# Performance work log

Hardware: AMD Instinct MI355X
Metric: run time of the kernel (lower is better)

## Reference

```python
import jax, jax.numpy as jnp
import numpy as np

EMBED_DIM = 768
NUM_HEADS = 12
HEAD_DIM = EMBED_DIM // NUM_HEADS
SCALE = HEAD_DIM ** -0.5
EPS = 1e-5


def _layernorm(x, g, b):
    m = jnp.mean(x, axis=-1, keepdims=True)
    v = jnp.mean(jnp.square(x - m), axis=-1, keepdims=True)
    return (x - m) * jax.lax.rsqrt(v + EPS) * g + b


def setup_inputs() -> dict:
    key = jax.random.key(0)
    ks = jax.random.split(key, 8)
    B, N, D, Hd = 16, 1024, EMBED_DIM, HEAD_DIM
    x = jax.random.normal(ks[0], (B, N, D), dtype=jnp.float32)
    W_qkv = jax.random.normal(ks[1], (D, 3 * D), dtype=jnp.float32) * (D ** -0.5)
    b_qkv = jnp.zeros((3 * D,), dtype=jnp.float32)
    W_proj = jax.random.normal(ks[2], (D, D), dtype=jnp.float32) * (D ** -0.5)
    b_proj = jnp.zeros((D,), dtype=jnp.float32)
    return {
        "x": x,
        "ln_g": jnp.ones((D,), jnp.float32), "ln_b": jnp.zeros((D,), jnp.float32),
        "W_qkv": W_qkv, "b_qkv": b_qkv,
        "qn_g": jnp.ones((Hd,), jnp.float32), "qn_b": jnp.zeros((Hd,), jnp.float32),
        "kn_g": jnp.ones((Hd,), jnp.float32), "kn_b": jnp.zeros((Hd,), jnp.float32),
        "W_proj": W_proj, "b_proj": b_proj,
    }


def reference(x, ln_g, ln_b, W_qkv, b_qkv, qn_g, qn_b, kn_g, kn_b, W_proj, b_proj):
    B, N, D = x.shape
    H, Hd = NUM_HEADS, HEAD_DIM
    xn = _layernorm(x, ln_g, ln_b)                      # qkv_norm (pre-LN of embed_dim)
    qkv = xn @ W_qkv + b_qkv                            # [B,N,3D]
    qkv = qkv.reshape(B, N, 3, H, Hd)
    q = jnp.transpose(qkv[:, :, 0], (0, 2, 1, 3))       # [B,H,N,Hd]
    k = jnp.transpose(qkv[:, :, 1], (0, 2, 1, 3))
    v = jnp.transpose(qkv[:, :, 2], (0, 2, 1, 3))
    q = _layernorm(q, qn_g, qn_b)                       # per-head QK LayerNorm
    k = _layernorm(k, kn_g, kn_b)
    attn = jnp.einsum("bhnd,bhmd->bhnm", q, k) * SCALE
    attn = jax.nn.softmax(attn, axis=-1)
    out = jnp.einsum("bhnm,bhmd->bhnd", attn, v)        # [B,H,N,Hd]
    out = jnp.transpose(out, (0, 2, 1, 3)).reshape(B, N, D)
    return out @ W_proj + b_proj
```

## Files before the change

kernel.cpp:

```cpp
#include <hip/hip_runtime.h>

typedef _Float16 half8 __attribute__((ext_vector_type(8)));
typedef _Float16 half4 __attribute__((ext_vector_type(4)));
typedef _Float16 half2v __attribute__((ext_vector_type(2)));
typedef float f32x4 __attribute__((ext_vector_type(4)));

#define B_    16
#define N_    1024
#define D_    768
#define H_    12
#define M_    (B_ * N_)
#define QKVN_ 2304
#define EPS_  1e-5f
#define QS_   0.18033688011112042f

__device__ __forceinline__ float exp2_fast(float x) {
#if __has_builtin(__builtin_amdgcn_exp2f)
    return __builtin_amdgcn_exp2f(x);
#else
    return __builtin_exp2f(x);
#endif
}

__device__ __forceinline__ size_t pk(int t16, int kc, int lg, int p, int e) {
    return ((size_t)(t16 * 24 + kc) * 4 + lg) * 128 + p * 8 + e;
}

__global__ __launch_bounds__(256) void convert_w(const float* __restrict__ Wqkv,
                                                 const float* __restrict__ Wproj,
                                                 _Float16* __restrict__ wqkv_p,
                                                 _Float16* __restrict__ wproj_p) {
    __shared__ float T[64][65];
    int t = blockIdx.x;
    const float* W; _Float16* O; int NW, k0, n0;
    if (t < 432) { W = Wqkv;  O = wqkv_p;  NW = QKVN_; k0 = (t % 12) * 64; n0 = (t / 12) * 64; }
    else { t -= 432; W = Wproj; O = wproj_p; NW = D_;  k0 = (t % 12) * 64; n0 = (t / 12) * 64; }
    int c = threadIdx.x & 63, r4 = threadIdx.x >> 6;
#pragma unroll
    for (int i = 0; i < 16; ++i) {
        int k = i * 4 + r4;
        T[c][k] = W[(size_t)(k0 + k) * NW + n0 + c];
    }
    __syncthreads();
    int g = threadIdx.x >> 5, s2 = threadIdx.x & 31;
    int ntl = g & 3, kcl = g >> 2;
    int nt = (n0 >> 4) + ntl, kc = (k0 >> 5) + kcl;
#pragma unroll
    for (int hh = 0; hh < 2; ++hh) {
        int s = s2 + hh * 32;
        int lg = s >> 4, p = s & 15;
        half8 v;
#pragma unroll
        for (int e = 0; e < 8; ++e)
            v[e] = (_Float16)T[ntl * 16 + p][kcl * 32 + lg * 8 + e];
        *(half8*)&O[((size_t)(nt * 24 + kc) * 4 + lg) * 128 + p * 8] = v;
    }
}

__global__ __launch_bounds__(256) void ln_embed(const float* __restrict__ x,
                                                const float* __restrict__ g,
                                                const float* __restrict__ bb,
                                                _Float16* __restrict__ xp) {
    int row = blockIdx.x;
    int tid = threadIdx.x;
    const float2* xr = (const float2*)(x + (size_t)row * D_);
    float2 v0 = xr[tid];
    float2 v1 = make_float2(0.f, 0.f);
    if (tid < 128) v1 = xr[256 + tid];
    float s = v0.x + v0.y + v1.x + v1.y;
    float q = v0.x * v0.x + v0.y * v0.y + v1.x * v1.x + v1.y * v1.y;
#pragma unroll
    for (int m = 32; m >= 1; m >>= 1) {
        s += __shfl_xor(s, m);
        q += __shfl_xor(q, m);
    }
    __shared__ float ss[4], qq[4];
    int wave = tid >> 6;
    if ((tid & 63) == 0) { ss[wave] = s; qq[wave] = q; }
    __syncthreads();
    float S = ss[0] + ss[1] + ss[2] + ss[3];
    float Q = qq[0] + qq[1] + qq[2] + qq[3];
    float mean = S * (1.f / 768.f);
    float var  = Q * (1.f / 768.f) - mean * mean;
    float rstd = rsqrtf(var + EPS_);
    const float2* g2 = (const float2*)g;
    const float2* b2 = (const float2*)bb;
    int mt = row >> 4, p = row & 15;
    {
        int d0 = 2 * tid;
        float2 ga = g2[tid], ba = b2[tid];
        half2v w;
        w[0] = (_Float16)((v0.x - mean) * rstd * ga.x + ba.x);
        w[1] = (_Float16)((v0.y - mean) * rstd * ga.y + ba.y);
        *(half2v*)&xp[pk(mt, d0 >> 5, (d0 >> 3) & 3, p, d0 & 7)] = w;
    }
    if (tid < 128) {
        int d0 = 512 + 2 * tid;
        float2 ga = g2[256 + tid], ba = b2[256 + tid];
        half2v w;
        w[0] = (_Float16)((v1.x - mean) * rstd * ga.x + ba.x);
        w[1] = (_Float16)((v1.y - mean) * rstd * ga.y + ba.y);
        *(half2v*)&xp[pk(mt, d0 >> 5, (d0 >> 3) & 3, p, d0 & 7)] = w;
    }
}

__global__ __launch_bounds__(256, 3) void gemm_qkv(const _Float16* __restrict__ Ap,
                                                   const _Float16* __restrict__ Bp,
                                                   const float* __restrict__ bias,
                                                   const float* __restrict__ qn_g,
                                                   const float* __restrict__ qn_b,
                                                   const float* __restrict__ kn_g,
                                                   const float* __restrict__ kn_b,
                                                   _Float16* __restrict__ qo,
                                                   _Float16* __restrict__ ko,
                                                   _Float16* __restrict__ vt) {
    int xcd = blockIdx.x & 7, loc = blockIdx.x >> 3;
    int mt0 = (xcd * 16 + (loc & 15)) * 8;
    int nt0 = (loc >> 4) * 8;
    int tid = threadIdx.x;
    int wave = tid >> 6, lane = tid & 63;
    int wm = wave >> 1, wn = wave & 1;
    int lg = lane >> 4, l15 = lane & 15;

    const _Float16* pa[4];
    const _Float16* pb[4];
#pragma unroll
    for (int i = 0; i < 4; ++i) {
        pa[i] = Ap + (size_t)(mt0 + wm * 4 + i) * 12288 + lane * 8;
        pb[i] = Bp + (size_t)(nt0 + wn * 4 + i) * 12288 + lane * 8;
    }
    f32x4 acc[4][4] = {};
    half8 a0[4], b0[4], a1[4], b1[4], a2[4], b2[4];
    auto ld = [&](half8 (&a)[4], half8 (&b)[4], int t) {
        int off = t * 512;
#pragma unroll
        for (int i = 0; i < 4; ++i) {
            a[i] = *(const half8*)(pa[i] + off);
            b[i] = *(const half8*)(pb[i] + off);
        }
    };
    auto mm = [&](half8 (&a)[4], half8 (&b)[4]) {
#pragma unroll
        for (int mi = 0; mi < 4; ++mi)
#pragma unroll
            for (int ni = 0; ni < 4; ++ni)
                acc[mi][ni] = __builtin_amdgcn_mfma_f32_16x16x32_f16(a[mi], b[ni], acc[mi][ni], 0, 0, 0);
    };
    ld(a0, b0, 0); ld(a1, b1, 1);
    for (int tt = 0; tt < 8; ++tt) {
        ld(a2, b2, 3 * tt + 2);
        mm(a0, b0);
        if (tt < 7) ld(a0, b0, 3 * tt + 3);
        mm(a1, b1);
        if (tt < 7) ld(a1, b1, 3 * tt + 4);
        mm(a2, b2);
    }

    int m0 = mt0 * 16, n0 = nt0 * 16;
    int col0 = n0 + wn * 64;
    int s = col0 / 768;
    int hcol = (col0 % 768) >> 6;
    float qkvb[4];
#pragma unroll
    for (int ni = 0; ni < 4; ++ni) qkvb[ni] = bias[col0 + ni * 16 + l15];

    if (s == 2) {
#pragma unroll
        for (int mi = 0; mi < 4; ++mi) {
            int r0 = m0 + wm * 64 + mi * 16 + lg * 4;
            int bidx = r0 >> 10, pos = r0 & 1023;
            int kvblk = pos >> 5, h = (pos >> 4) & 1, lgR = (pos >> 2) & 3;
            size_t vbase = ((size_t)(bidx * H_ + hcol) * 32 + kvblk) * 4;
#pragma unroll
            for (int ni = 0; ni < 4; ++ni) {
                half4 h4;
#pragma unroll
                for (int j = 0; j < 4; ++j) h4[j] = (_Float16)(acc[mi][ni][j] + qkvb[ni]);
                *(half4*)&vt[(vbase + ni) * 512 + lgR * 128 + l15 * 8 + h * 4] = h4;
            }
        }
    } else {
        const float* gg = (s == 0) ? qn_g : kn_g;
        const float* bb = (s == 0) ? qn_b : kn_b;
        float gv[4], bv[4];
#pragma unroll
        for (int ni = 0; ni < 4; ++ni) { gv[ni] = gg[ni * 16 + l15]; bv[ni] = bb[ni * 16 + l15]; }
#pragma unroll
        for (int mi = 0; mi < 4; ++mi) {
#pragma unroll
            for (int j = 0; j < 4; ++j) {
                float v[4];
                float sm = 0.f, sq = 0.f;
#pragma unroll
                for (int ni = 0; ni < 4; ++ni) {
                    v[ni] = acc[mi][ni][j] + qkvb[ni];
                    sm += v[ni];
                    sq += v[ni] * v[ni];
                }
#pragma unroll
                for (int msk = 1; msk < 16; msk <<= 1) {
                    sm += __shfl_xor(sm, msk);
                    sq += __shfl_xor(sq, msk);
                }
                float mean = sm * (1.f / 64.f);
                float var  = sq * (1.f / 64.f) - mean * mean;
                float rstd = rsqrtf(var + EPS_);
                int row = m0 + wm * 64 + mi * 16 + lg * 4 + j;
                int bidx = row >> 10, pos = row & 1023;
                if (s == 0) {
                    size_t rbase = ((size_t)(bidx * H_ + hcol) * 1024 + pos) * 64;
#pragma unroll
                    for (int ni = 0; ni < 4; ++ni) {
                        float o = (v[ni] - mean) * rstd * gv[ni] + bv[ni];
                        qo[rbase + ni * 16 + l15] = (_Float16)(o * QS_);
                    }
                } else {
                    int kvblk = pos >> 5, nh = (pos >> 4) & 1, l15R = pos & 15;
                    size_t base2 = ((size_t)(bidx * H_ + hcol) * 32 + kvblk) * 4 + nh * 2;
#pragma unroll
                    for (int ni = 0; ni < 4; ++ni) {
                        float o = (v[ni] - mean) * rstd * gv[ni] + bv[ni];
                        int ks = ni >> 1, lgR = ((ni & 1) << 1) | (l15 >> 3), elem = l15 & 7;
                        ko[(base2 + ks) * 512 + lgR * 128 + l15R * 8 + elem] = (_Float16)o;
                    }
                }
            }
        }
    }
}

struct KV {
    half8 kf[2][2];
    half8 vf[4];
};

__device__ __forceinline__ void ldKV(KV& s, const _Float16* kp, const _Float16* vp, int kvblk) {
    const _Float16* kb = kp + (size_t)kvblk * 2048;
#pragma unroll
    for (int nh = 0; nh < 2; ++nh)
#pragma unroll
        for (int ks = 0; ks < 2; ++ks)
            s.kf[nh][ks] = *(const half8*)(kb + (nh * 2 + ks) * 512);
    const _Float16* vb = vp + (size_t)kvblk * 2048;
#pragma unroll
    for (int di = 0; di < 4; ++di)
        s.vf[di] = *(const half8*)(vb + di * 512);
}

__device__ __forceinline__ void blockKV(const KV& s, const half8 (&qf)[4][2],
                                        f32x4 (&oacc)[4][4], f32x4 (&lacc)[4],
                                        half8 ones) {
#pragma unroll
    for (int mi = 0; mi < 4; ++mi) {
        f32x4 a0 = {}, a1 = {};
#pragma unroll
        for (int ks = 0; ks < 2; ++ks) {
            a0 = __builtin_amdgcn_mfma_f32_16x16x32_f16(s.kf[0][ks], qf[mi][ks], a0, 0, 0, 0);
            a1 = __builtin_amdgcn_mfma_f32_16x16x32_f16(s.kf[1][ks], qf[mi][ks], a1, 0, 0, 0);
        }
        half8 pf;
#pragma unroll
        for (int j = 0; j < 4; ++j) {
            pf[j]     = (_Float16)exp2_fast(a0[j]);
            pf[j + 4] = (_Float16)exp2_fast(a1[j]);
        }
        lacc[mi] = __builtin_amdgcn_mfma_f32_16x16x32_f16(ones, pf, lacc[mi], 0, 0, 0);
#pragma unroll
        for (int di = 0; di < 4; ++di)
            oacc[mi][di] = __builtin_amdgcn_mfma_f32_16x16x32_f16(s.vf[di], pf, oacc[mi][di], 0, 0, 0);
    }
}

__global__ __launch_bounds__(128, 2) void attn(const _Float16* __restrict__ qg,
                                               const _Float16* __restrict__ kg,
                                               const _Float16* __restrict__ vtg,
                                               _Float16* __restrict__ op) {
    int bphys = blockIdx.x;
    int jj = (bphys & 7) * 192 + (bphys >> 3);
    int bh = jj >> 3, qt = jj & 7;
    int b = bh / H_, h = bh % H_;
    int tid = threadIdx.x;
    int wid = tid >> 6, lane = tid & 63;
    int lg = lane >> 4, l15 = lane & 15;
    size_t base = (size_t)bh << 10;
    int qw0 = qt * 128 + wid * 64;

    const _Float16* qrow = qg + (base + qw0 + l15) * 64 + lg * 8;
    half8 qf[4][2];
#pragma unroll
    for (int mi = 0; mi < 4; ++mi)
#pragma unroll
        for (int ks = 0; ks < 2; ++ks)
            qf[mi][ks] = *(const half8*)(qrow + mi * 1024 + ks * 32);

    const _Float16* kp = kg + (size_t)bh * 65536 + lane * 8;
    const _Float16* vp = vtg + (size_t)bh * 65536 + lane * 8;

    half8 ones;
#pragma unroll
    for (int i = 0; i < 8; ++i) ones[i] = (_Float16)1.0f;

    f32x4 oacc[4][4] = {};
    f32x4 lacc[4] = {};

    KV s0, s1;
    ldKV(s0, kp, vp, 0);
    for (int t = 0; t < 16; ++t) {
        ldKV(s1, kp, vp, (2 * t + 1) & 31);
        blockKV(s0, qf, oacc, lacc, ones);
        ldKV(s0, kp, vp, (2 * t + 2) & 31);
        blockKV(s1, qf, oacc, lacc, ones);
    }

#pragma unroll
    for (int mi = 0; mi < 4; ++mi) {
        float inv = 1.f / lacc[mi][0];
        int mt = b * 64 + (qw0 >> 4) + mi;
#pragma unroll
        for (int di = 0; di < 4; ++di) {
            half4 h4;
#pragma unroll
            for (int j = 0; j < 4; ++j) h4[j] = (_Float16)(oacc[mi][di][j] * inv);
            *(half4*)&op[pk(mt, 2 * h + (di >> 1), (di & 1) * 2 + (lg >> 1), l15, (lg & 1) * 4)] = h4;
        }
    }
}

__global__ __launch_bounds__(256, 3) void gemm_proj(const _Float16* __restrict__ Ap,
                                                    const _Float16* __restrict__ Bp,
                                                    const float* __restrict__ bias,
                                                    float* __restrict__ out) {
    int xcd = blockIdx.x & 7, loc = blockIdx.x >> 3;
    int mt0 = (xcd * 16 + (loc & 15)) * 8;
    int nt0 = (loc >> 4) * 8;
    int tid = threadIdx.x;
    int wave = tid >> 6, lane = tid & 63;
    int wm = wave >> 1, wn = wave & 1;
    int lg = lane >> 4, l15 = lane & 15;

    const _Float16* pa[4];
    const _Float16* pb[4];
#pragma unroll
    for (int i = 0; i < 4; ++i) {
        pa[i] = Ap + (size_t)(mt0 + wm * 4 + i) * 12288 + lane * 8;
        pb[i] = Bp + (size_t)(nt0 + wn * 4 + i) * 12288 + lane * 8;
    }
    f32x4 acc[4][4] = {};
    half8 a0[4], b0[4], a1[4], b1[4], a2[4], b2[4];
    auto ld = [&](half8 (&a)[4], half8 (&b)[4], int t) {
        int off = t * 512;
#pragma unroll
        for (int i = 0; i < 4; ++i) {
            a[i] = *(const half8*)(pa[i] + off);
            b[i] = *(const half8*)(pb[i] + off);
        }
    };
    auto mm = [&](half8 (&a)[4], half8 (&b)[4]) {
#pragma unroll
        for (int mi = 0; mi < 4; ++mi)
#pragma unroll
            for (int ni = 0; ni < 4; ++ni)
                acc[mi][ni] = __builtin_amdgcn_mfma_f32_16x16x32_f16(a[mi], b[ni], acc[mi][ni], 0, 0, 0);
    };
    ld(a0, b0, 0); ld(a1, b1, 1);
    for (int tt = 0; tt < 8; ++tt) {
        ld(a2, b2, 3 * tt + 2);
        mm(a0, b0);
        if (tt < 7) ld(a0, b0, 3 * tt + 3);
        mm(a1, b1);
        if (tt < 7) ld(a1, b1, 3 * tt + 4);
        mm(a2, b2);
    }

    int m0 = mt0 * 16, n0 = nt0 * 16;
#pragma unroll
    for (int mi = 0; mi < 4; ++mi)
#pragma unroll
        for (int ni = 0; ni < 4; ++ni) {
            int col = n0 + wn * 64 + ni * 16 + l15;
            float bv = bias[col];
#pragma unroll
            for (int j = 0; j < 4; ++j) {
                int row = m0 + wm * 64 + mi * 16 + lg * 4 + j;
                out[(size_t)row * D_ + col] = acc[mi][ni][j] + bv;
            }
        }
}

extern "C" void kernel_launch(void* const* d_in, const int* in_sizes, int n_in,
                              void* d_out, int out_size, void* d_ws, size_t ws_size,
                              hipStream_t stream) {
    const float* x      = (const float*)d_in[0];
    const float* ln_g   = (const float*)d_in[1];
    const float* ln_b   = (const float*)d_in[2];
    const float* W_qkv  = (const float*)d_in[3];
    const float* b_qkv  = (const float*)d_in[4];
    const float* qn_g   = (const float*)d_in[5];
    const float* qn_b   = (const float*)d_in[6];
    const float* kn_g   = (const float*)d_in[7];
    const float* kn_b   = (const float*)d_in[8];
    const float* W_proj = (const float*)d_in[9];
    const float* b_proj = (const float*)d_in[10];
    float* out = (float*)d_out;
    char* ws = (char*)d_ws;

    constexpr size_t XN_SZ    = (size_t)M_ * D_ * 2;
    constexpr size_t WQKVT_SZ = (size_t)QKVN_ * D_ * 2;
    constexpr size_t WPROJT_SZ= (size_t)D_ * D_ * 2;
    constexpr size_t HEAD_SZ  = (size_t)B_ * H_ * N_ * 64 * 2;

    _Float16* xn_p   = (_Float16*)(ws);
    _Float16* wqkv_p = (_Float16*)(ws + XN_SZ);
    _Float16* wproj_p= (_Float16*)(ws + XN_SZ + WQKVT_SZ);
    _Float16* qb     = (_Float16*)(ws + XN_SZ + WQKVT_SZ + WPROJT_SZ);
    _Float16* kb     = (_Float16*)((char*)qb + HEAD_SZ);
    _Float16* vtb    = (_Float16*)((char*)kb + HEAD_SZ);
    _Float16* ao_p   = xn_p;

    convert_w<<<576, 256, 0, stream>>>(W_qkv, W_proj, wqkv_p, wproj_p);
    ln_embed<<<M_, 256, 0, stream>>>(x, ln_g, ln_b, xn_p);
    gemm_qkv<<<M_ / 128 * (QKVN_ / 128), 256, 0, stream>>>(xn_p, wqkv_p, b_qkv,
                                                           qn_g, qn_b, kn_g, kn_b,
                                                           qb, kb, vtb);
    attn<<<B_ * H_ * (N_ / 128), 128, 0, stream>>>(qb, kb, vtb, ao_p);
    gemm_proj<<<M_ / 128 * (D_ / 128), 256, 0, stream>>>(ao_p, wproj_p, b_proj, out);
}
```

Baseline: 201.6 us.

## Stage GEMM tiles through LDS with async global-to-LDS loads and triple buffering

Both GEMMs move from per-wave direct global loads to 256x128 block tiles staged in shared memory through global_load_lds, with a three-buffer pipeline, explicit barriers and vmcnt waits. Each block now has 8 waves, so A and B fragments are loaded once and shared across waves rather than fetched by every wave from global memory. The activation and weight packed layouts are reorganised into 64-wide K tiles so each staging copy is contiguous, and the writers (LN, attention output, weight conversion) are changed to match. The hand-scheduled waits and barriers carry correctness risk, and the larger blocks lower occupancy.

```diff
diff --git a/kernel.cpp b/kernel.cpp
--- a/kernel.cpp
+++ b/kernel.cpp
@@ -22,8 +22,18 @@
 #endif
 }
 
-__device__ __forceinline__ size_t pk(int t16, int kc, int lg, int p, int e) {
-    return ((size_t)(t16 * 24 + kc) * 4 + lg) * 128 + p * 8 + e;
+__device__ __forceinline__ void gl16(const _Float16* g, _Float16* l) {
+    __builtin_amdgcn_global_load_lds((const __attribute__((address_space(1))) void*)g,
+                                     (__attribute__((address_space(3))) void*)l, 16, 0, 0);
+}
+
+#define BARR() asm volatile("s_barrier" ::: "memory")
+#define VM6()  asm volatile("s_waitcnt vmcnt(6)" ::: "memory")
+
+__device__ __forceinline__ size_t aidx(int row, int d) {
+    return ((size_t)((row >> 8) * 12 + (d >> 6))) * 16384
+         + ((((row >> 4) & 15) * 2) + ((d >> 5) & 1)) * 512
+         + (((d >> 3) & 3)) * 128 + (row & 15) * 8 + (d & 7);
 }
 
 __global__ __launch_bounds__(256) void convert_w(const float* __restrict__ Wqkv,
@@ -42,18 +52,19 @@
         T[c][k] = W[(size_t)(k0 + k) * NW + n0 + c];
     }
     __syncthreads();
-    int g = threadIdx.x >> 5, s2 = threadIdx.x & 31;
-    int ntl = g & 3, kcl = g >> 2;
-    int nt = (n0 >> 4) + ntl, kc = (k0 >> 5) + kcl;
-#pragma unroll
-    for (int hh = 0; hh < 2; ++hh) {
-        int s = s2 + hh * 32;
-        int lg = s >> 4, p = s & 15;
+    int kt = k0 >> 6;
+    int ntile = n0 >> 7;
+    int t16base = (n0 >> 4) & 7;
+#pragma unroll
+    for (int it = 0; it < 2; ++it) {
+        int g = it * 256 + threadIdx.x;
+        int t16l = g >> 7, ksub = (g >> 6) & 1, lgI = (g >> 4) & 3, p = g & 15;
         half8 v;
 #pragma unroll
         for (int e = 0; e < 8; ++e)
-            v[e] = (_Float16)T[ntl * 16 + p][kcl * 32 + lg * 8 + e];
-        *(half8*)&O[((size_t)(nt * 24 + kc) * 4 + lg) * 128 + p * 8] = v;
+            v[e] = (_Float16)T[t16l * 16 + p][ksub * 32 + lgI * 8 + e];
+        *(half8*)&O[((size_t)(ntile * 12 + kt)) * 8192 +
+                    ((t16base + t16l) * 2 + ksub) * 512 + lgI * 128 + p * 8] = v;
     }
 }
 
@@ -85,14 +96,13 @@
     float rstd = rsqrtf(var + EPS_);
     const float2* g2 = (const float2*)g;
     const float2* b2 = (const float2*)bb;
-    int mt = row >> 4, p = row & 15;
     {
         int d0 = 2 * tid;
         float2 ga = g2[tid], ba = b2[tid];
         half2v w;
         w[0] = (_Float16)((v0.x - mean) * rstd * ga.x + ba.x);
         w[1] = (_Float16)((v0.y - mean) * rstd * ga.y + ba.y);
-        *(half2v*)&xp[pk(mt, d0 >> 5, (d0 >> 3) & 3, p, d0 & 7)] = w;
+        *(half2v*)&xp[aidx(row, d0)] = w;
     }
     if (tid < 128) {
         int d0 = 512 + 2 * tid;
@@ -100,11 +110,11 @@
         half2v w;
         w[0] = (_Float16)((v1.x - mean) * rstd * ga.x + ba.x);
         w[1] = (_Float16)((v1.y - mean) * rstd * ga.y + ba.y);
-        *(half2v*)&xp[pk(mt, d0 >> 5, (d0 >> 3) & 3, p, d0 & 7)] = w;
-    }
-}
-
-__global__ __launch_bounds__(256, 3) void gemm_qkv(const _Float16* __restrict__ Ap,
+        *(half2v*)&xp[aidx(row, d0)] = w;
+    }
+}
+
+__global__ __launch_bounds__(512, 2) void gemm_qkv(const _Float16* __restrict__ Ap,
                                                    const _Float16* __restrict__ Bp,
                                                    const float* __restrict__ bias,
                                                    const float* __restrict__ qn_g,
@@ -114,49 +124,73 @@
                                                    _Float16* __restrict__ qo,
                                                    _Float16* __restrict__ ko,
                                                    _Float16* __restrict__ vt) {
+    __shared__ _Float16 lds[3 * 24576];
     int xcd = blockIdx.x & 7, loc = blockIdx.x >> 3;
-    int mt0 = (xcd * 16 + (loc & 15)) * 8;
-    int nt0 = (loc >> 4) * 8;
+    int mt = xcd * 8 + (loc & 7);
+    int nb = loc >> 3;
     int tid = threadIdx.x;
-    int wave = tid >> 6, lane = tid & 63;
-    int wm = wave >> 1, wn = wave & 1;
+    int wid = tid >> 6, lane = tid & 63;
+    int wm = wid >> 1, wn = wid & 1;
     int lg = lane >> 4, l15 = lane & 15;
 
-    const _Float16* pa[4];
-    const _Float16* pb[4];
-#pragma unroll
-    for (int i = 0; i < 4; ++i) {
-        pa[i] = Ap + (size_t)(mt0 + wm * 4 + i) * 12288 + lane * 8;
-        pb[i] = Bp + (size_t)(nt0 + wn * 4 + i) * 12288 + lane * 8;
-    }
+    const _Float16* Abase = Ap + (size_t)mt * (12 * 16384) + wid * 512 + lane * 8;
+    const _Float16* Bbase = Bp + (size_t)nb * (12 * 8192) + wid * 512 + lane * 8;
+
     f32x4 acc[4][4] = {};
-    half8 a0[4], b0[4], a1[4], b1[4], a2[4], b2[4];
-    auto ld = [&](half8 (&a)[4], half8 (&b)[4], int t) {
-        int off = t * 512;
-#pragma unroll
-        for (int i = 0; i < 4; ++i) {
-            a[i] = *(const half8*)(pa[i] + off);
-            b[i] = *(const half8*)(pb[i] + off);
-        }
-    };
-    auto mm = [&](half8 (&a)[4], half8 (&b)[4]) {
-#pragma unroll
-        for (int mi = 0; mi < 4; ++mi)
-#pragma unroll
-            for (int ni = 0; ni < 4; ++ni)
-                acc[mi][ni] = __builtin_amdgcn_mfma_f32_16x16x32_f16(a[mi], b[ni], acc[mi][ni], 0, 0, 0);
-    };
-    ld(a0, b0, 0); ld(a1, b1, 1);
-    for (int tt = 0; tt < 8; ++tt) {
-        ld(a2, b2, 3 * tt + 2);
-        mm(a0, b0);
-        if (tt < 7) ld(a0, b0, 3 * tt + 3);
-        mm(a1, b1);
-        if (tt < 7) ld(a1, b1, 3 * tt + 4);
-        mm(a2, b2);
-    }
-
-    int m0 = mt0 * 16, n0 = nt0 * 16;
+    half8 a[4], b[4];
+
+#define STG_A(buf, kt, pass) gl16(Abase + (kt) * 16384 + (pass) * 4096, \
+                                  &lds[(buf) * 24576 + (pass) * 4096 + wid * 512])
+#define STG_B(buf, kt, pass) gl16(Bbase + (kt) * 8192 + (pass) * 4096, \
+                                  &lds[(buf) * 24576 + 16384 + (pass) * 4096 + wid * 512])
+#define DSRD(buf, ks)                                                                 \
+    _Pragma("unroll")                                                                 \
+    for (int mi = 0; mi < 4; ++mi)                                                    \
+        a[mi] = *(const half8*)&lds[(buf) * 24576 + ((wm * 4 + mi) * 2 + (ks)) * 512 + lane * 8]; \
+    _Pragma("unroll")                                                                 \
+    for (int ni = 0; ni < 4; ++ni)                                                    \
+        b[ni] = *(const half8*)&lds[(buf) * 24576 + 16384 + ((wn * 4 + ni) * 2 + (ks)) * 512 + lane * 8];
+#define MM16()                                                                        \
+    _Pragma("unroll")                                                                 \
+    for (int mi = 0; mi < 4; ++mi)                                                    \
+        _Pragma("unroll")                                                             \
+        for (int ni = 0; ni < 4; ++ni)                                                \
+            acc[mi][ni] = __builtin_amdgcn_mfma_f32_16x16x32_f16(a[mi], b[ni], acc[mi][ni], 0, 0, 0);
+
+#pragma unroll
+    for (int u = 0; u < 2; ++u) {
+        STG_A(u, u, 0); STG_A(u, u, 1); STG_B(u, u, 0);
+        STG_A(u, u, 2); STG_A(u, u, 3); STG_B(u, u, 1);
+    }
+    VM6();
+    BARR();
+
+    for (int t = 0; t < 12; ++t) {
+        int buf = t % 3;
+        int nbuf = (t + 2) % 3;
+        int ktw = (t >= 10) ? (t - 10) : (t + 2);
+        DSRD(buf, 0);
+        STG_A(nbuf, ktw, 0); STG_A(nbuf, ktw, 1); STG_B(nbuf, ktw, 0);
+        BARR();
+        __builtin_amdgcn_s_setprio(1);
+        MM16();
+        __builtin_amdgcn_s_setprio(0);
+        BARR();
+        DSRD(buf, 1);
+        STG_A(nbuf, ktw, 2); STG_A(nbuf, ktw, 3); STG_B(nbuf, ktw, 1);
+        VM6();
+        BARR();
+        __builtin_amdgcn_s_setprio(1);
+        MM16();
+        __builtin_amdgcn_s_setprio(0);
+        BARR();
+    }
+#undef STG_A
+#undef STG_B
+#undef DSRD
+#undef MM16
+
+    int m0 = mt * 256, n0 = nb * 128;
     int col0 = n0 + wn * 64;
     int s = col0 / 768;
     int hcol = (col0 % 768) >> 6;
@@ -315,64 +349,91 @@
 #pragma unroll
     for (int mi = 0; mi < 4; ++mi) {
         float inv = 1.f / lacc[mi][0];
-        int mt = b * 64 + (qw0 >> 4) + mi;
+        int row0 = b * 1024 + qw0 + mi * 16;
+        int mtv = row0 >> 8, t16 = (row0 >> 4) & 15;
 #pragma unroll
         for (int di = 0; di < 4; ++di) {
             half4 h4;
 #pragma unroll
             for (int j = 0; j < 4; ++j) h4[j] = (_Float16)(oacc[mi][di][j] * inv);
-            *(half4*)&op[pk(mt, 2 * h + (di >> 1), (di & 1) * 2 + (lg >> 1), l15, (lg & 1) * 4)] = h4;
-        }
-    }
-}
-
-__global__ __launch_bounds__(256, 3) void gemm_proj(const _Float16* __restrict__ Ap,
+            size_t o = ((size_t)(mtv * 12 + h)) * 16384 + (t16 * 2 + (di >> 1)) * 512
+                     + ((di & 1) * 2 + (lg >> 1)) * 128 + l15 * 8 + (lg & 1) * 4;
+            *(half4*)&op[o] = h4;
+        }
+    }
+}
+
+__global__ __launch_bounds__(512, 2) void gemm_proj(const _Float16* __restrict__ Ap,
                                                     const _Float16* __restrict__ Bp,
                                                     const float* __restrict__ bias,
                                                     float* __restrict__ out) {
+    __shared__ _Float16 lds[3 * 24576];
     int xcd = blockIdx.x & 7, loc = blockIdx.x >> 3;
-    int mt0 = (xcd * 16 + (loc & 15)) * 8;
-    int nt0 = (loc >> 4) * 8;
+    int mt = xcd * 8 + (loc & 7);
+    int nb = loc >> 3;
     int tid = threadIdx.x;
-    int wave = tid >> 6, lane = tid & 63;
-    int wm = wave >> 1, wn = wave & 1;
+    int wid = tid >> 6, lane = tid & 63;
+    int wm = wid >> 1, wn = wid & 1;
     int lg = lane >> 4, l15 = lane & 15;
 
-    const _Float16* pa[4];
-    const _Float16* pb[4];
-#pragma unroll
-    for (int i = 0; i < 4; ++i) {
-        pa[i] = Ap + (size_t)(mt0 + wm * 4 + i) * 12288 + lane * 8;
-        pb[i] = Bp + (size_t)(nt0 + wn * 4 + i) * 12288 + lane * 8;
-    }
+    const _Float16* Abase = Ap + (size_t)mt * (12 * 16384) + wid * 512 + lane * 8;
+    const _Float16* Bbase = Bp + (size_t)nb * (12 * 8192) + wid * 512 + lane * 8;
+
     f32x4 acc[4][4] = {};
-    half8 a0[4], b0[4], a1[4], b1[4], a2[4], b2[4];
-    auto ld = [&](half8 (&a)[4], half8 (&b)[4], int t) {
-        int off = t * 512;
-#pragma unroll
-        for (int i = 0; i < 4; ++i) {
-            a[i] = *(const half8*)(pa[i] + off);
-            b[i] = *(const half8*)(pb[i] + off);
-        }
-    };
-    auto mm = [&](half8 (&a)[4], half8 (&b)[4]) {
-#pragma unroll
-        for (int mi = 0; mi < 4; ++mi)
-#pragma unroll
-            for (int ni = 0; ni < 4; ++ni)
-                acc[mi][ni] = __builtin_amdgcn_mfma_f32_16x16x32_f16(a[mi], b[ni], acc[mi][ni], 0, 0, 0);
-    };
-    ld(a0, b0, 0); ld(a1, b1, 1);
-    for (int tt = 0; tt < 8; ++tt) {
-        ld(a2, b2, 3 * tt + 2);
-        mm(a0, b0);
-        if (tt < 7) ld(a0, b0, 3 * tt + 3);
-        mm(a1, b1);
-        if (tt < 7) ld(a1, b1, 3 * tt + 4);
-        mm(a2, b2);
-    }
-
-    int m0 = mt0 * 16, n0 = nt0 * 16;
+    half8 a[4], b[4];
+
+#define STG_A(buf, kt, pass) gl16(Abase + (kt) * 16384 + (pass) * 4096, \
+                                  &lds[(buf) * 24576 + (pass) * 4096 + wid * 512])
+#define STG_B(buf, kt, pass) gl16(Bbase + (kt) * 8192 + (pass) * 4096, \
+                                  &lds[(buf) * 24576 + 16384 + (pass) * 4096 + wid * 512])
+#define DSRD(buf, ks)                                                                 \
+    _Pragma("unroll")                                                                 \
+    for (int mi = 0; mi < 4; ++mi)                                                    \
+        a[mi] = *(const half8*)&lds[(buf) * 24576 + ((wm * 4 + mi) * 2 + (ks)) * 512 + lane * 8]; \
+    _Pragma("unroll")                                                                 \
+    for (int ni = 0; ni < 4; ++ni)                                                    \
+        b[ni] = *(const half8*)&lds[(buf) * 24576 + 16384 + ((wn * 4 + ni) * 2 + (ks)) * 512 + lane * 8];
+#define MM16()                                                                        \
+    _Pragma("unroll")                                                                 \
+    for (int mi = 0; mi < 4; ++mi)                                                    \
+        _Pragma("unroll")                                                             \
+        for (int ni = 0; ni < 4; ++ni)                                                \
+            acc[mi][ni] = __builtin_amdgcn_mfma_f32_16x16x32_f16(a[mi], b[ni], acc[mi][ni], 0, 0, 0);
+
+#pragma unroll
+    for (int u = 0; u < 2; ++u) {
+        STG_A(u, u, 0); STG_A(u, u, 1); STG_B(u, u, 0);
+        STG_A(u, u, 2); STG_A(u, u, 3); STG_B(u, u, 1);
+    }
+    VM6();
+    BARR();
+
+    for (int t = 0; t < 12; ++t) {
+        int buf = t % 3;
+        int nbuf = (t + 2) % 3;
+        int ktw = (t >= 10) ? (t - 10) : (t + 2);
+        DSRD(buf, 0);
+        STG_A(nbuf, ktw, 0); STG_A(nbuf, ktw, 1); STG_B(nbuf, ktw, 0);
+        BARR();
+        __builtin_amdgcn_s_setprio(1);
+        MM16();
+        __builtin_amdgcn_s_setprio(0);
+        BARR();
+        DSRD(buf, 1);
+        STG_A(nbuf, ktw, 2); STG_A(nbuf, ktw, 3); STG_B(nbuf, ktw, 1);
+        VM6();
+        BARR();
+        __builtin_amdgcn_s_setprio(1);
+        MM16();
+        __builtin_amdgcn_s_setprio(0);
+        BARR();
+    }
+#undef STG_A
+#undef STG_B
+#undef DSRD
+#undef MM16
+
+    int m0 = mt * 256, n0 = nb * 128;
 #pragma unroll
     for (int mi = 0; mi < 4; ++mi)
 #pragma unroll
@@ -419,9 +480,9 @@
 
     convert_w<<<576, 256, 0, stream>>>(W_qkv, W_proj, wqkv_p, wproj_p);
     ln_embed<<<M_, 256, 0, stream>>>(x, ln_g, ln_b, xn_p);
-    gemm_qkv<<<M_ / 128 * (QKVN_ / 128), 256, 0, stream>>>(xn_p, wqkv_p, b_qkv,
-                                                           qn_g, qn_b, kn_g, kn_b,
-                                                           qb, kb, vtb);
+    gemm_qkv<<<(M_ / 256) * (QKVN_ / 128), 512, 0, stream>>>(xn_p, wqkv_p, b_qkv,
+                                                             qn_g, qn_b, kn_g, kn_b,
+                                                             qb, kb, vtb);
     attn<<<B_ * H_ * (N_ / 128), 128, 0, stream>>>(qb, kb, vtb, ao_p);
-    gemm_proj<<<M_ / 128 * (D_ / 128), 256, 0, stream>>>(ao_p, wproj_p, b_proj, out);
-}
+    gemm_proj<<<(M_ / 256) * (D_ / 128), 512, 0, stream>>>(ao_p, wproj_p, b_proj, out);
+}
```

Result: slower. 208.0 us (+3.2%).

## Re-tile packed fp16 layouts for block-contiguous GEMM loads and transposed QK epilogue

Applied to the files above, without the earlier changes.

Changes the packed layouts of the normalized activations, weights and attention output so that each 128-row/128-col block's K-slices are contiguous in 64-wide K tiles. The GEMMs switch from triple to double register buffering over 24 K-steps. For Q/K the QKV GEMM swaps MFMA operands so each lane holds a row's head dims, which cuts the per-row layernorm shuffle reduction to two xor steps and allows vectorized half4 stores. Q is now written in a blocked layout that attention reads directly. The intent is better memory locality and a cheaper epilogue, at the risk of less load latency hiding. There is also a redundant scalar store before the half4 store.

```diff
diff --git a/kernel.cpp b/kernel.cpp
--- a/kernel.cpp
+++ b/kernel.cpp
@@ -22,8 +22,10 @@
 #endif
 }
 
-__device__ __forceinline__ size_t pk(int t16, int kc, int lg, int p, int e) {
-    return ((size_t)(t16 * 24 + kc) * 4 + lg) * 128 + p * 8 + e;
+__device__ __forceinline__ size_t aidx(int row, int d) {
+    return ((size_t)((row >> 8) * 12 + (d >> 6))) * 16384
+         + ((((row >> 4) & 15) * 2) + ((d >> 5) & 1)) * 512
+         + (((d >> 3) & 3)) * 128 + (row & 15) * 8 + (d & 7);
 }
 
 __global__ __launch_bounds__(256) void convert_w(const float* __restrict__ Wqkv,
@@ -42,18 +44,19 @@
         T[c][k] = W[(size_t)(k0 + k) * NW + n0 + c];
     }
     __syncthreads();
-    int g = threadIdx.x >> 5, s2 = threadIdx.x & 31;
-    int ntl = g & 3, kcl = g >> 2;
-    int nt = (n0 >> 4) + ntl, kc = (k0 >> 5) + kcl;
-#pragma unroll
-    for (int hh = 0; hh < 2; ++hh) {
-        int s = s2 + hh * 32;
-        int lg = s >> 4, p = s & 15;
+    int kt = k0 >> 6;
+    int ntile = n0 >> 7;
+    int t16base = (n0 >> 4) & 7;
+#pragma unroll
+    for (int it = 0; it < 2; ++it) {
+        int g = it * 256 + threadIdx.x;
+        int t16l = g >> 7, ksub = (g >> 6) & 1, lgI = (g >> 4) & 3, p = g & 15;
         half8 v;
 #pragma unroll
         for (int e = 0; e < 8; ++e)
-            v[e] = (_Float16)T[ntl * 16 + p][kcl * 32 + lg * 8 + e];
-        *(half8*)&O[((size_t)(nt * 24 + kc) * 4 + lg) * 128 + p * 8] = v;
+            v[e] = (_Float16)T[t16l * 16 + p][ksub * 32 + lgI * 8 + e];
+        *(half8*)&O[((size_t)(ntile * 12 + kt)) * 8192 +
+                    ((t16base + t16l) * 2 + ksub) * 512 + lgI * 128 + p * 8] = v;
     }
 }
 
@@ -85,14 +88,13 @@
     float rstd = rsqrtf(var + EPS_);
     const float2* g2 = (const float2*)g;
     const float2* b2 = (const float2*)bb;
-    int mt = row >> 4, p = row & 15;
     {
         int d0 = 2 * tid;
         float2 ga = g2[tid], ba = b2[tid];
         half2v w;
         w[0] = (_Float16)((v0.x - mean) * rstd * ga.x + ba.x);
         w[1] = (_Float16)((v0.y - mean) * rstd * ga.y + ba.y);
-        *(half2v*)&xp[pk(mt, d0 >> 5, (d0 >> 3) & 3, p, d0 & 7)] = w;
+        *(half2v*)&xp[aidx(row, d0)] = w;
     }
     if (tid < 128) {
         int d0 = 512 + 2 * tid;
@@ -100,12 +102,12 @@
         half2v w;
         w[0] = (_Float16)((v1.x - mean) * rstd * ga.x + ba.x);
         w[1] = (_Float16)((v1.y - mean) * rstd * ga.y + ba.y);
-        *(half2v*)&xp[pk(mt, d0 >> 5, (d0 >> 3) & 3, p, d0 & 7)] = w;
-    }
-}
-
-__global__ __launch_bounds__(256, 3) void gemm_qkv(const _Float16* __restrict__ Ap,
-                                                   const _Float16* __restrict__ Bp,
+        *(half2v*)&xp[aidx(row, d0)] = w;
+    }
+}
+
+__global__ __launch_bounds__(256, 3) void gemm_qkv(const _Float16* __restrict__ Xp,
+                                                   const _Float16* __restrict__ Wp,
                                                    const float* __restrict__ bias,
                                                    const float* __restrict__ qn_g,
                                                    const float* __restrict__ qn_b,
@@ -115,56 +117,76 @@
                                                    _Float16* __restrict__ ko,
                                                    _Float16* __restrict__ vt) {
     int xcd = blockIdx.x & 7, loc = blockIdx.x >> 3;
-    int mt0 = (xcd * 16 + (loc & 15)) * 8;
-    int nt0 = (loc >> 4) * 8;
+    int mblk = xcd * 16 + (loc & 15);
+    int nb = loc >> 4;
     int tid = threadIdx.x;
-    int wave = tid >> 6, lane = tid & 63;
-    int wm = wave >> 1, wn = wave & 1;
+    int wid = tid >> 6, lane = tid & 63;
+    int wm = wid >> 1, wn = wid & 1;
     int lg = lane >> 4, l15 = lane & 15;
-
-    const _Float16* pa[4];
-    const _Float16* pb[4];
-#pragma unroll
-    for (int i = 0; i < 4; ++i) {
-        pa[i] = Ap + (size_t)(mt0 + wm * 4 + i) * 12288 + lane * 8;
-        pb[i] = Bp + (size_t)(nt0 + wn * 4 + i) * 12288 + lane * 8;
-    }
+    bool isV = (nb >= 12);
+
+    const _Float16* pw = Wp + (size_t)nb * 98304 + (wn * 4) * 1024 + lane * 8;
+    const _Float16* px = Xp + (size_t)(mblk >> 1) * 196608 +
+                         ((mblk & 1) * 8 + wm * 4) * 1024 + lane * 8;
+
     f32x4 acc[4][4] = {};
-    half8 a0[4], b0[4], a1[4], b1[4], a2[4], b2[4];
-    auto ld = [&](half8 (&a)[4], half8 (&b)[4], int t) {
-        int off = t * 512;
+    half8 xa0[4], wb0[4], xa1[4], wb1[4];
+    auto ld = [&](half8 (&xa)[4], half8 (&wb)[4], int t) {
+        int kt = t >> 1, ks = t & 1;
+        size_t offW = (size_t)kt * 8192 + ks * 512;
+        size_t offX = (size_t)kt * 16384 + ks * 512;
 #pragma unroll
         for (int i = 0; i < 4; ++i) {
-            a[i] = *(const half8*)(pa[i] + off);
-            b[i] = *(const half8*)(pb[i] + off);
+            xa[i] = *(const half8*)(px + i * 1024 + offX);
+            wb[i] = *(const half8*)(pw + i * 1024 + offW);
         }
     };
-    auto mm = [&](half8 (&a)[4], half8 (&b)[4]) {
+    auto mmQK = [&](half8 (&xa)[4], half8 (&wb)[4]) {
+#pragma unroll
+        for (int ni = 0; ni < 4; ++ni)
+#pragma unroll
+            for (int mi = 0; mi < 4; ++mi)
+                acc[ni][mi] = __builtin_amdgcn_mfma_f32_16x16x32_f16(wb[ni], xa[mi], acc[ni][mi], 0, 0, 0);
+    };
+    auto mmV = [&](half8 (&xa)[4], half8 (&wb)[4]) {
 #pragma unroll
         for (int mi = 0; mi < 4; ++mi)
 #pragma unroll
             for (int ni = 0; ni < 4; ++ni)
-                acc[mi][ni] = __builtin_amdgcn_mfma_f32_16x16x32_f16(a[mi], b[ni], acc[mi][ni], 0, 0, 0);
+                acc[mi][ni] = __builtin_amdgcn_mfma_f32_16x16x32_f16(xa[mi], wb[ni], acc[mi][ni], 0, 0, 0);
     };
-    ld(a0, b0, 0); ld(a1, b1, 1);
-    for (int tt = 0; tt < 8; ++tt) {
-        ld(a2, b2, 3 * tt + 2);
-        mm(a0, b0);
-        if (tt < 7) ld(a0, b0, 3 * tt + 3);
-        mm(a1, b1);
-        if (tt < 7) ld(a1, b1, 3 * tt + 4);
-        mm(a2, b2);
-    }
-
-    int m0 = mt0 * 16, n0 = nt0 * 16;
-    int col0 = n0 + wn * 64;
-    int s = col0 / 768;
-    int hcol = (col0 % 768) >> 6;
-    float qkvb[4];
-#pragma unroll
-    for (int ni = 0; ni < 4; ++ni) qkvb[ni] = bias[col0 + ni * 16 + l15];
-
-    if (s == 2) {
+
+    ld(xa0, wb0, 0);
+    if (isV) {
+        for (int tt = 0; tt < 11; ++tt) {
+            ld(xa1, wb1, 2 * tt + 1);
+            mmV(xa0, wb0);
+            ld(xa0, wb0, 2 * tt + 2);
+            mmV(xa1, wb1);
+        }
+        ld(xa1, wb1, 23);
+        mmV(xa0, wb0);
+        mmV(xa1, wb1);
+    } else {
+        for (int tt = 0; tt < 11; ++tt) {
+            ld(xa1, wb1, 2 * tt + 1);
+            mmQK(xa0, wb0);
+            ld(xa0, wb0, 2 * tt + 2);
+            mmQK(xa1, wb1);
+        }
+        ld(xa1, wb1, 23);
+        mmQK(xa0, wb0);
+        mmQK(xa1, wb1);
+    }
+
+    int m0 = mblk * 128;
+    int col0 = nb * 128 + wn * 64;
+
+    if (isV) {
+        int hcol = (col0 % 768) >> 6;
+        float qkvb[4];
+#pragma unroll
+        for (int ni = 0; ni < 4; ++ni) qkvb[ni] = bias[col0 + ni * 16 + l15];
 #pragma unroll
         for (int mi = 0; mi < 4; ++mi) {
             int r0 = m0 + wm * 64 + mi * 16 + lg * 4;
@@ -180,50 +202,56 @@
             }
         }
     } else {
+        int s = col0 / 768;
+        int hcol = (col0 % 768) >> 6;
         const float* gg = (s == 0) ? qn_g : kn_g;
-        const float* bb = (s == 0) ? qn_b : kn_b;
-        float gv[4], bv[4];
-#pragma unroll
-        for (int ni = 0; ni < 4; ++ni) { gv[ni] = gg[ni * 16 + l15]; bv[ni] = bb[ni * 16 + l15]; }
+        const float* bv = (s == 0) ? qn_b : kn_b;
+        _Float16* dst = (s == 0) ? qo : ko;
+        float4 g4[4], b4[4], bi4[4];
+#pragma unroll
+        for (int ni = 0; ni < 4; ++ni) {
+            g4[ni]  = *(const float4*)&gg[ni * 16 + lg * 4];
+            b4[ni]  = *(const float4*)&bv[ni * 16 + lg * 4];
+            bi4[ni] = *(const float4*)&bias[col0 + ni * 16 + lg * 4];
+        }
+        int posbase = m0 + wm * 64;
+        int bidx = posbase >> 10;
+        size_t bh0 = (size_t)(bidx * H_ + hcol) * 65536;
+        float scl = (s == 0) ? QS_ : 1.0f;
 #pragma unroll
         for (int mi = 0; mi < 4; ++mi) {
-#pragma unroll
-            for (int j = 0; j < 4; ++j) {
-                float v[4];
-                float sm = 0.f, sq = 0.f;
-#pragma unroll
-                for (int ni = 0; ni < 4; ++ni) {
-                    v[ni] = acc[mi][ni][j] + qkvb[ni];
-                    sm += v[ni];
-                    sq += v[ni] * v[ni];
+            float vv[4][4];
+            float sm = 0.f, sq = 0.f;
+#pragma unroll
+            for (int ni = 0; ni < 4; ++ni)
+#pragma unroll
+                for (int j = 0; j < 4; ++j) {
+                    float bvj = (j == 0) ? bi4[ni].x : (j == 1) ? bi4[ni].y : (j == 2) ? bi4[ni].z : bi4[ni].w;
+                    float v = acc[ni][mi][j] + bvj;
+                    vv[ni][j] = v;
+                    sm += v;
+                    sq += v * v;
                 }
-#pragma unroll
-                for (int msk = 1; msk < 16; msk <<= 1) {
-                    sm += __shfl_xor(sm, msk);
-                    sq += __shfl_xor(sq, msk);
+            sm += __shfl_xor(sm, 16); sq += __shfl_xor(sq, 16);
+            sm += __shfl_xor(sm, 32); sq += __shfl_xor(sq, 32);
+            float mean = sm * (1.f / 64.f);
+            float var  = sq * (1.f / 64.f) - mean * mean;
+            float rstd = rsqrtf(var + EPS_) * scl;
+            float meanb = mean;
+            int posL = ((posbase & 1023) + mi * 16);
+            size_t obase = bh0 + (size_t)(posL >> 5) * 2048 + ((posL >> 4) & 1) * 1024
+                         + l15 * 8 + (lg & 1) * 4;
+#pragma unroll
+            for (int ni = 0; ni < 4; ++ni) {
+                half4 h4;
+#pragma unroll
+                for (int j = 0; j < 4; ++j) {
+                    float gj = (j == 0) ? g4[ni].x : (j == 1) ? g4[ni].y : (j == 2) ? g4[ni].z : g4[ni].w;
+                    float bj = (j == 0) ? b4[ni].x : (j == 1) ? b4[ni].y : (j == 2) ? b4[ni].z : b4[ni].w;
+                    h4[j] = (_Float16)((vv[ni][j] - meanb) * rstd * gj + bj * scl);
                 }
-                float mean = sm * (1.f / 64.f);
-                float var  = sq * (1.f / 64.f) - mean * mean;
-                float rstd = rsqrtf(var + EPS_);
-                int row = m0 + wm * 64 + mi * 16 + lg * 4 + j;
-                int bidx = row >> 10, pos = row & 1023;
-                if (s == 0) {
-                    size_t rbase = ((size_t)(bidx * H_ + hcol) * 1024 + pos) * 64;
-#pragma unroll
-                    for (int ni = 0; ni < 4; ++ni) {
-                        float o = (v[ni] - mean) * rstd * gv[ni] + bv[ni];
-                        qo[rbase + ni * 16 + l15] = (_Float16)(o * QS_);
-                    }
-                } else {
-                    int kvblk = pos >> 5, nh = (pos >> 4) & 1, l15R = pos & 15;
-                    size_t base2 = ((size_t)(bidx * H_ + hcol) * 32 + kvblk) * 4 + nh * 2;
-#pragma unroll
-                    for (int ni = 0; ni < 4; ++ni) {
-                        float o = (v[ni] - mean) * rstd * gv[ni] + bv[ni];
-                        int ks = ni >> 1, lgR = ((ni & 1) << 1) | (l15 >> 3), elem = l15 & 7;
-                        ko[(base2 + ks) * 512 + lgR * 128 + l15R * 8 + elem] = (_Float16)o;
-                    }
-                }
+                dst[obase + (ni >> 1) * 512 + (((ni & 1) << 1) | (lg >> 1)) * 128] = h4[0];
+                *(half4*)&dst[obase + (ni >> 1) * 512 + (((ni & 1) << 1) | (lg >> 1)) * 128] = h4;
             }
         }
     }
@@ -282,16 +310,15 @@
     int tid = threadIdx.x;
     int wid = tid >> 6, lane = tid & 63;
     int lg = lane >> 4, l15 = lane & 15;
-    size_t base = (size_t)bh << 10;
     int qw0 = qt * 128 + wid * 64;
 
-    const _Float16* qrow = qg + (base + qw0 + l15) * 64 + lg * 8;
+    const _Float16* qp2 = qg + (size_t)bh * 65536 + (size_t)(qw0 >> 5) * 2048 + lane * 8;
     half8 qf[4][2];
 #pragma unroll
     for (int mi = 0; mi < 4; ++mi)
 #pragma unroll
         for (int ks = 0; ks < 2; ++ks)
-            qf[mi][ks] = *(const half8*)(qrow + mi * 1024 + ks * 32);
+            qf[mi][ks] = *(const half8*)(qp2 + (mi >> 1) * 2048 + (mi & 1) * 1024 + ks * 512);
 
     const _Float16* kp = kg + (size_t)bh * 65536 + lane * 8;
     const _Float16* vp = vtg + (size_t)bh * 65536 + lane * 8;
@@ -315,64 +342,67 @@
 #pragma unroll
     for (int mi = 0; mi < 4; ++mi) {
         float inv = 1.f / lacc[mi][0];
-        int mt = b * 64 + (qw0 >> 4) + mi;
+        int row0 = b * 1024 + qw0 + mi * 16;
+        int mtv = row0 >> 8, t16 = (row0 >> 4) & 15;
 #pragma unroll
         for (int di = 0; di < 4; ++di) {
             half4 h4;
 #pragma unroll
             for (int j = 0; j < 4; ++j) h4[j] = (_Float16)(oacc[mi][di][j] * inv);
-            *(half4*)&op[pk(mt, 2 * h + (di >> 1), (di & 1) * 2 + (lg >> 1), l15, (lg & 1) * 4)] = h4;
+            size_t o = ((size_t)(mtv * 12 + h)) * 16384 + (t16 * 2 + (di >> 1)) * 512
+                     + ((di & 1) * 2 + (lg >> 1)) * 128 + l15 * 8 + (lg & 1) * 4;
+            *(half4*)&op[o] = h4;
         }
     }
 }
 
 __global__ __launch_bounds__(256, 3) void gemm_proj(const _Float16* __restrict__ Ap,
-                                                    const _Float16* __restrict__ Bp,
+                                                    const _Float16* __restrict__ Wp,
                                                     const float* __restrict__ bias,
                                                     float* __restrict__ out) {
     int xcd = blockIdx.x & 7, loc = blockIdx.x >> 3;
-    int mt0 = (xcd * 16 + (loc & 15)) * 8;
-    int nt0 = (loc >> 4) * 8;
+    int mblk = xcd * 16 + (loc & 15);
+    int nb = loc >> 4;
     int tid = threadIdx.x;
-    int wave = tid >> 6, lane = tid & 63;
-    int wm = wave >> 1, wn = wave & 1;
+    int wid = tid >> 6, lane = tid & 63;
+    int wm = wid >> 1, wn = wid & 1;
     int lg = lane >> 4, l15 = lane & 15;
 
-    const _Float16* pa[4];
-    const _Float16* pb[4];
-#pragma unroll
-    for (int i = 0; i < 4; ++i) {
-        pa[i] = Ap + (size_t)(mt0 + wm * 4 + i) * 12288 + lane * 8;
-        pb[i] = Bp + (size_t)(nt0 + wn * 4 + i) * 12288 + lane * 8;
-    }
+    const _Float16* pw = Wp + (size_t)nb * 98304 + (wn * 4) * 1024 + lane * 8;
+    const _Float16* px = Ap + (size_t)(mblk >> 1) * 196608 +
+                         ((mblk & 1) * 8 + wm * 4) * 1024 + lane * 8;
+
     f32x4 acc[4][4] = {};
-    half8 a0[4], b0[4], a1[4], b1[4], a2[4], b2[4];
-    auto ld = [&](half8 (&a)[4], half8 (&b)[4], int t) {
-        int off = t * 512;
+    half8 xa0[4], wb0[4], xa1[4], wb1[4];
+    auto ld = [&](half8 (&xa)[4], half8 (&wb)[4], int t) {
+        int kt = t >> 1, ks = t & 1;
+        size_t offW = (size_t)kt * 8192 + ks * 512;
+        size_t offX = (size_t)kt * 16384 + ks * 512;
 #pragma unroll
         for (int i = 0; i < 4; ++i) {
-            a[i] = *(const half8*)(pa[i] + off);
-            b[i] = *(const half8*)(pb[i] + off);
+            xa[i] = *(const half8*)(px + i * 1024 + offX);
+            wb[i] = *(const half8*)(pw + i * 1024 + offW);
         }
     };
-    auto mm = [&](half8 (&a)[4], half8 (&b)[4]) {
+    auto mm = [&](half8 (&xa)[4], half8 (&wb)[4]) {
 #pragma unroll
         for (int mi = 0; mi < 4; ++mi)
 #pragma unroll
             for (int ni = 0; ni < 4; ++ni)
-                acc[mi][ni] = __builtin_amdgcn_mfma_f32_16x16x32_f16(a[mi], b[ni], acc[mi][ni], 0, 0, 0);
+                acc[mi][ni] = __builtin_amdgcn_mfma_f32_16x16x32_f16(xa[mi], wb[ni], acc[mi][ni], 0, 0, 0);
     };
-    ld(a0, b0, 0); ld(a1, b1, 1);
-    for (int tt = 0; tt < 8; ++tt) {
-        ld(a2, b2, 3 * tt + 2);
-        mm(a0, b0);
-        if (tt < 7) ld(a0, b0, 3 * tt + 3);
-        mm(a1, b1);
-        if (tt < 7) ld(a1, b1, 3 * tt + 4);
-        mm(a2, b2);
-    }
-
-    int m0 = mt0 * 16, n0 = nt0 * 16;
+    ld(xa0, wb0, 0);
+    for (int tt = 0; tt < 11; ++tt) {
+        ld(xa1, wb1, 2 * tt + 1);
+        mm(xa0, wb0);
+        ld(xa0, wb0, 2 * tt + 2);
+        mm(xa1, wb1);
+    }
+    ld(xa1, wb1, 23);
+    mm(xa0, wb0);
+    mm(xa1, wb1);
+
+    int m0 = mblk * 128, n0 = nb * 128;
 #pragma unroll
     for (int mi = 0; mi < 4; ++mi)
 #pragma unroll
@@ -419,9 +449,9 @@
 
     convert_w<<<576, 256, 0, stream>>>(W_qkv, W_proj, wqkv_p, wproj_p);
     ln_embed<<<M_, 256, 0, stream>>>(x, ln_g, ln_b, xn_p);
-    gemm_qkv<<<M_ / 128 * (QKVN_ / 128), 256, 0, stream>>>(xn_p, wqkv_p, b_qkv,
-                                                           qn_g, qn_b, kn_g, kn_b,
-                                                           qb, kb, vtb);
+    gemm_qkv<<<(M_ / 128) * (QKVN_ / 128), 256, 0, stream>>>(xn_p, wqkv_p, b_qkv,
+                                                             qn_g, qn_b, kn_g, kn_b,
+                                                             qb, kb, vtb);
     attn<<<B_ * H_ * (N_ / 128), 128, 0, stream>>>(qb, kb, vtb, ao_p);
-    gemm_proj<<<M_ / 128 * (D_ / 128), 256, 0, stream>>>(ao_p, wproj_p, b_proj, out);
-}
+    gemm_proj<<<(M_ / 128) * (D_ / 128), 256, 0, stream>>>(ao_p, wproj_p, b_proj, out);
+}
```

Result: faster. 190.1 us (-5.7%).
